# Performance work log

Hardware: AMD Instinct MI355X
Metric: run time of the kernel (lower is better)

## Reference

```python
import jax, jax.numpy as jnp
from jax import lax
import numpy as np

BATCH, SEQ_LEN, ENC_IN, C_OUT = 16, 512, 32, 32
N_ORDER = 256           # window_size
MULTISCALE = (1, 2, 4)
MODES = min(32, SEQ_LEN // 2)  # = 32


def make_hippo(N, dt):
    """HiPPO-LegT transition, bilinear (Tustin) discretization, Legendre eval matrix."""
    Q = np.arange(N, dtype=np.float64)
    R = (2 * Q + 1)[:, None]
    j, i = np.meshgrid(Q, Q)
    A = np.where(i < j, -1.0, (-1.0) ** (i - j + 1)) * R
    B = (-1.0) ** Q[:, None] * R                      # [N,1]
    I = np.eye(N)
    M = I - (dt / 2.0) * A
    Ad = np.linalg.solve(M, I + (dt / 2.0) * A)
    Bd = np.linalg.solve(M, dt * B).squeeze(-1)       # [N]
    vals = np.arange(0.0, 1.0, dt)
    x = 1.0 - 2.0 * vals
    P = np.zeros((N, len(vals)))
    P[0] = 1.0
    if N > 1:
        P[1] = x
    for n in range(1, N - 1):
        P[n + 1] = ((2 * n + 1) * x * P[n] - n * P[n - 1]) / (n + 1)
    E = P.T                                           # [len(vals), N]
    return Ad.astype(np.float32), Bd.astype(np.float32), E.astype(np.float32)


def setup_inputs():
    key = jax.random.key(0)
    ks = jax.random.split(key, 12)
    inp = {}
    inp['x_enc'] = jax.random.normal(ks[0], (BATCH, SEQ_LEN, ENC_IN), jnp.float32)
    inp['x_mark_enc'] = jax.random.normal(ks[1], (BATCH, SEQ_LEN, 4), jnp.float32)
    inp['x_dec'] = jax.random.normal(ks[2], (BATCH, SEQ_LEN, ENC_IN), jnp.float32)
    inp['x_mark_dec'] = jax.random.normal(ks[3], (BATCH, SEQ_LEN, 4), jnp.float32)
    inp['affine_weight'] = jnp.ones((1, 1, ENC_IN), jnp.float32)
    inp['affine_bias'] = jnp.zeros((1, 1, ENC_IN), jnp.float32)
    scale = 1.0 / (N_ORDER * N_ORDER)
    for s in range(3):
        inp[f'wr{s}'] = scale * jax.random.uniform(ks[4 + 2 * s], (N_ORDER, N_ORDER, MODES), jnp.float32)
        inp[f'wi{s}'] = scale * jax.random.uniform(ks[5 + 2 * s], (N_ORDER, N_ORDER, MODES), jnp.float32)
    inp['mlp_w'] = 0.1 * jax.random.normal(ks[10], (1, 3), jnp.float32)
    inp['mlp_b'] = jnp.zeros((1,), jnp.float32)
    inp['proj_w'] = 0.02 * jax.random.normal(ks[11], (ENC_IN, C_OUT), jnp.float32)
    inp['proj_b'] = jnp.zeros((C_OUT,), jnp.float32)
    for s, m in enumerate(MULTISCALE):
        A, Bv, E = make_hippo(N_ORDER, 1.0 / SEQ_LEN / m)
        inp[f'A{s}'] = jnp.asarray(A)
        inp[f'Bv{s}'] = jnp.asarray(Bv)
        inp[f'E{s}'] = jnp.asarray(E)
    return inp


def _hippo_scan(x, A, Bv):
    # x: [B, L, C] -> cs: [L, B, C, N]; c_t = A c_{t-1} + B f_t (applied on last dim)
    B_, L, C = x.shape
    c0 = jnp.zeros((B_, C, A.shape[0]), x.dtype)
    At = A.T
    def step(c, f):                      # f: [B, C]
        c = c @ At + f[..., None] * Bv
        return c, c
    _, cs = lax.scan(step, c0, jnp.transpose(x, (1, 0, 2)))
    return cs


def _spectral_conv(xc, wr, wi):
    # xc: [B, C, N, L]; keep first MODES rfft bins, complex channel mix over N, irfft
    L = xc.shape[-1]
    xf = jnp.fft.rfft(xc)                                # [B,C,N,L//2+1] complex64
    W = (wr + 1j * wi).astype(jnp.complex64)             # [N,N,MODES]
    out = jnp.einsum('bjix,iox->bjox', xf[..., :MODES], W)
    out_ft = jnp.pad(out, ((0, 0), (0, 0), (0, 0), (0, L // 2 + 1 - MODES)))
    return jnp.fft.irfft(out_ft, n=L)                    # [B,C,N,L]


def _forward(x_enc, affine_weight, affine_bias, specs, mlp_w, mlp_b, proj_w, proj_b, hippos):
    means = lax.stop_gradient(jnp.mean(x_enc, axis=1, keepdims=True))
    xc = x_enc - means
    stdev = lax.stop_gradient(jnp.sqrt(jnp.var(xc, axis=1, keepdims=True) + 1e-5))
    x = xc / stdev
    x = x * affine_weight + affine_bias                  # [B, L, C]
    pred_len = SEQ_LEN
    decs = []
    for (wr, wi), (A, Bv, E) in zip(specs, hippos):
        # multiscale slice x[:, -m*pred_len:] clips to full seq_len since pred_len==seq_len
        cs = _hippo_scan(x, A, Bv)                       # [L,B,C,N]
        x_in_c = jnp.transpose(cs, (1, 2, 3, 0))         # [B,C,N,L]
        out1 = _spectral_conv(x_in_c, wr, wi)            # [B,C,N,L]
        x_dec_c = out1[..., pred_len - 1]                # [B,C,N]
        dec = x_dec_c @ E[-pred_len:, :].T               # [B,C,pred_len]
        decs.append(dec)
    stacked = jnp.stack(decs, axis=-1)                   # [B,C,P,3]
    y = stacked @ mlp_w[0] + mlp_b[0]                    # Linear(3,1) + squeeze -> [B,C,P]
    y = jnp.transpose(y, (0, 2, 1))                      # [B,P,C]
    y = (y - affine_bias) / (affine_weight + 1e-10)
    y = y * stdev + means
    return y @ proj_w + proj_b                           # OutputBlock: per-step channel projection


def reference(x_enc, x_mark_enc, x_dec, x_mark_dec, affine_weight, affine_bias,
              wr0, wi0, wr1, wi1, wr2, wi2, mlp_w, mlp_b, proj_w, proj_b,
              A0, Bv0, E0, A1, Bv1, E1, A2, Bv2, E2):
    specs = [(wr0, wi0), (wr1, wi1), (wr2, wi2)]
    hippos = [(A0, Bv0, E0), (A1, Bv1, E1), (A2, Bv2, E2)]
    return _forward(x_enc, affine_weight, affine_bias, specs, mlp_w, mlp_b, proj_w, proj_b, hippos)
```

## Files before the change

### kernel.cpp

```cpp
#include <hip/hip_runtime.h>
#include <math.h>

#define SEQ 512
#define NORD 256
#define MODES 32
#define KBIG (NORD*MODES*2)
#define PI_F 3.14159265358979323846f

typedef _Float16 half8 __attribute__((ext_vector_type(8)));
typedef float floatx4 __attribute__((ext_vector_type(4)));


struct GJob {
  const float* A; const float* B; float* C; const float* scale_ptr;
  int M, N, lda, k0, k1, atomic;
};
struct GJobs { GJob j[6]; };

__global__ __launch_bounds__(256) void gemm32_k(GJobs P) {
  GJob jb = P.j[blockIdx.z];
  int col0 = blockIdx.x * 32;
  int row0 = blockIdx.y * 32;
  if (row0 >= jb.M || col0 >= jb.N) return;
  __shared__ float As[64][34];
  __shared__ float Bs[64][36];
  int tid = threadIdx.x;
  int tx = tid & 15, ty = tid >> 4;
  const float* A = jb.A; const float* B = jb.B;
  int M = jb.M, N = jb.N, lda = jb.lda;
  int kcA = (tid & 15) * 4, rA = tid >> 4;
  int ccB = (tid & 7) * 4, kkB = tid >> 3;
  int gr0 = row0 + rA, gr1 = row0 + rA + 16;
  const float4 z4 = make_float4(0.f, 0.f, 0.f, 0.f);
  float4 a0, a1, b0, b1;
  {
    int kb = jb.k0;
    a0 = (gr0 < M) ? *(const float4*)&A[(size_t)gr0 * lda + kb + kcA] : z4;
    a1 = (gr1 < M) ? *(const float4*)&A[(size_t)gr1 * lda + kb + kcA] : z4;
    b0 = *(const float4*)&B[(size_t)(kb + kkB) * N + col0 + ccB];
    b1 = *(const float4*)&B[(size_t)(kb + kkB + 32) * N + col0 + ccB];
  }
  float acc00 = 0.f, acc01 = 0.f, acc10 = 0.f, acc11 = 0.f;
  for (int kb = jb.k0; kb < jb.k1; kb += 64) {
    As[kcA+0][rA] = a0.x; As[kcA+1][rA] = a0.y; As[kcA+2][rA] = a0.z; As[kcA+3][rA] = a0.w;
    As[kcA+0][rA+16] = a1.x; As[kcA+1][rA+16] = a1.y; As[kcA+2][rA+16] = a1.z; As[kcA+3][rA+16] = a1.w;
    *(float4*)&Bs[kkB][ccB] = b0;
    *(float4*)&Bs[kkB+32][ccB] = b1;
    __syncthreads();
    if (kb + 64 < jb.k1) {
      int kn = kb + 64;
      a0 = (gr0 < M) ? *(const float4*)&A[(size_t)gr0 * lda + kn + kcA] : z4;
      a1 = (gr1 < M) ? *(const float4*)&A[(size_t)gr1 * lda + kn + kcA] : z4;
      b0 = *(const float4*)&B[(size_t)(kn + kkB) * N + col0 + ccB];
      b1 = *(const float4*)&B[(size_t)(kn + kkB + 32) * N + col0 + ccB];
    }
    #pragma unroll
    for (int k = 0; k < 64; k++) {
      float2 av = *(float2*)&As[k][ty * 2];
      float2 bv = *(float2*)&Bs[k][tx * 2];
      acc00 += av.x * bv.x; acc01 += av.x * bv.y;
      acc10 += av.y * bv.x; acc11 += av.y * bv.y;
    }
    __syncthreads();
  }
  float sc = jb.scale_ptr ? *jb.scale_ptr : 1.f;
  int gr = row0 + ty * 2, gc = col0 + tx * 2;
  float v00 = acc00 * sc, v01 = acc01 * sc, v10 = acc10 * sc, v11 = acc11 * sc;
  if (jb.atomic) {
    if (gr < M)     { atomicAdd(&jb.C[(size_t)gr * N + gc], v00);     atomicAdd(&jb.C[(size_t)gr * N + gc + 1], v01); }
    if (gr + 1 < M) { atomicAdd(&jb.C[(size_t)(gr+1) * N + gc], v10); atomicAdd(&jb.C[(size_t)(gr+1) * N + gc + 1], v11); }
  } else {
    if (gr < M)     { jb.C[(size_t)gr * N + gc] = v00;     jb.C[(size_t)gr * N + gc + 1] = v01; }
    if (gr + 1 < M) { jb.C[(size_t)(gr+1) * N + gc] = v10; jb.C[(size_t)(gr+1) * N + gc + 1] = v11; }
  }
}


__global__ __launch_bounds__(256) void prep_k(const float* A0, const float* A1, const float* A2,
                                              const float* B0, const float* B1, const float* B2,
                                              const float* E0, const float* E1, const float* E2,
                                              float* R, float* Kry, float* Et, float* Z) {
  long bid = blockIdx.x;
  if (bid < 768) {
    long idx = bid * 256 + threadIdx.x;
    int scl = (int)(idx >> 16);
    int r = (int)(idx & 65535);
    int m = r >> 8, i2 = r & 255;
    const float* A = scl == 0 ? A0 : (scl == 1 ? A1 : A2);
    R[(size_t)scl * 2 * 65536 + (size_t)m * 256 + i2] = A[(size_t)i2 * 256 + m];
  } else if (bid < 2304) {
    long idx = (bid - 768) * 256 + threadIdx.x;
    int scl = (int)(idx / 131072);
    int r = (int)(idx % 131072);
    int p = r >> 8, o = r & 255;
    const float* E; int rows;
    if (scl == 0) { E = E0; rows = 512; }
    else if (scl == 1) { E = E1; rows = 1024; }
    else { E = E2; rows = 2048; }
    int base = rows - 512;
    Et[(size_t)scl * 131072 + (size_t)o * 512 + p] = E[(size_t)(base + p) * 256 + o];
  } else if (bid < 2307) {
    int scl = (int)(bid - 2304);
    const float* B = scl == 0 ? B0 : (scl == 1 ? B1 : B2);
    Kry[(size_t)scl * 512 * 256 + threadIdx.x] = B[threadIdx.x];
  } else {
    long idx = (bid - 2307) * 256 + threadIdx.x;
    if (idx < 655360) Z[idx] = 0.f;
  }
}


__global__ __launch_bounds__(256) void revin_k(const float* __restrict__ x,
                                               const float* __restrict__ aw,
                                               const float* __restrict__ ab,
                                               float* __restrict__ F,
                                               float* __restrict__ stats) {
  int row = blockIdx.x;
  int b = row >> 5, c = row & 31;
  int tid = threadIdx.x;
  const float* xp = x + (size_t)b * SEQ * 32 + c;
  float v0 = xp[(size_t)tid * 32];
  float v1 = xp[(size_t)(tid + 256) * 32];
  float s = v0 + v1, s2 = v0 * v0 + v1 * v1;
  for (int off = 32; off; off >>= 1) {
    s  += __shfl_down(s,  off, 64);
    s2 += __shfl_down(s2, off, 64);
  }
  __shared__ float ws1[4], ws2[4];
  __shared__ float mean_s, istd_s;
  int wid = tid >> 6, lane = tid & 63;
  if (lane == 0) { ws1[wid] = s; ws2[wid] = s2; }
  __syncthreads();
  if (tid == 0) {
    float t1 = ws1[0] + ws1[1] + ws1[2] + ws1[3];
    float t2 = ws2[0] + ws2[1] + ws2[2] + ws2[3];
    float mean = t1 / 512.f;
    float var = t2 / 512.f - mean * mean;
    float sd = sqrtf(var + 1e-5f);
    mean_s = mean; istd_s = 1.f / sd;
    stats[row] = mean; stats[512 + row] = sd;
  }
  __syncthreads();
  float w = aw[c], bb = ab[c];
  float m = mean_s, is = istd_s;
  F[(size_t)row * SEQ + tid]       = (v0 - m) * is * w + bb;
  F[(size_t)row * SEQ + tid + 256] = (v1 - m) * is * w + bb;
}


__global__ __launch_bounds__(256) void qbuildA_k(const float* __restrict__ Kry,
                                                 float2* __restrict__ Pp, int s0) {
  int bg = blockIdx.x;
  int s = s0 + (bg >> 8);
  int r = bg & 255;
  int k = r & 31, c = r >> 5;
  const float* Kry_s = Kry + (size_t)s * 131072;
  float2* P = Pp + (size_t)s * 65536;
  int i = threadIdx.x;
  float ar = 0.f, ai = 0.f;
  const float step = 2.f * PI_F / 512.f;
  int m0 = c * 64;
  for (int mm = 0; mm < 64; mm++) {
    int m = m0 + mm;
    float kap = Kry_s[(size_t)m * 256 + i];
    float sn, cn; __sincosf(step * (float)((k * m) & 511), &sn, &cn);
    ar += kap * cn; ai -= kap * sn;
  }
  P[(size_t)(c * 32 + k) * 256 + i] = make_float2(ar, ai);
}

__global__ __launch_bounds__(256) void qbuildB_k(const float* __restrict__ Kry,
                                                 const float2* __restrict__ Pp,
                                                 _Float16* __restrict__ Qf, int s0) {
  int bg = blockIdx.x;
  int slab = bg >> 8;
  int s = s0 + slab;
  int r = bg & 255;
  int ig = r & 31, c = r >> 5;
  const float* Kry_s = Kry + (size_t)s * 131072;
  const float2* P = Pp + (size_t)s * 65536;
  uint4* Qd4 = (uint4*)(Qf + (size_t)slab * 8388608);
  int tid = threadIdx.x;
  int k = tid & 31, il = tid >> 5;
  int i = ig * 8 + il;
  __shared__ __align__(16) unsigned int buf[16 * 260];
  float ar = 0.f, ai = 0.f;
  for (int cp = 0; cp < c; cp++) {
    float2 p = P[(size_t)(cp * 32 + k) * 256 + i];
    ar += p.x; ai += p.y;
  }
  const float step = 2.f * PI_F / 512.f;
  int m0 = c * 64;
  int st_low = tid & 15;
  int part_base = tid >> 4;
  for (int mb = 0; mb < 64; mb += 16) {
    #pragma unroll
    for (int mm = 0; mm < 16; mm++) {
      int m = m0 + mb + mm;
      float kap = Kry_s[(size_t)m * 256 + i];
      float sn, cn; __sincosf(step * (float)((k * m) & 511), &sn, &cn);
      ar += kap * cn; ai -= kap * sn;
      int st = 511 - m;
      float sn2, cn2; __sincosf(step * (float)((k * st) & 511), &sn2, &cn2);
      float qr = ar * cn2 + ai * sn2;
      float qi = ai * cn2 - ar * sn2;
      qr = fminf(fmaxf(qr, -60000.f), 60000.f);
      qi = fminf(fmaxf(qi, -60000.f), 60000.f);
      _Float16 h0 = (_Float16)qr, h1 = (_Float16)qi;
      unsigned short u0, u1;
      __builtin_memcpy(&u0, &h0, 2); __builtin_memcpy(&u1, &h1, 2);
      buf[(st & 15) * 260 + il * 32 + k] = (unsigned int)u0 | ((unsigned int)u1 << 16);
    }
    __syncthreads();
    int st_base = 496 - m0 - mb;
    int st = st_base + st_low;
    size_t rowbase = (size_t)(st >> 4) * 512;
    #pragma unroll
    for (int p = 0; p < 4; p++) {
      int part = part_base + p * 16;
      int ilw = part >> 3, k4 = part & 7;
      int iw = ig * 8 + ilw;
      size_t g = (rowbase + (size_t)(iw * 2 + (k4 >> 2))) * 64
               + (size_t)((k4 & 3) * 16 + st_low);
      Qd4[g] = *(const uint4*)&buf[st_low * 260 + ilw * 32 + k4 * 4];
    }
    __syncthreads();
  }
}


__global__ __launch_bounds__(256) void wbigT_k(const float* wr0, const float* wi0,
                                               const float* wr1, const float* wi1,
                                               const float* wr2, const float* wi2,
                                               _Float16* __restrict__ Wt, int s0) {
  int bg = blockIdx.x;
  int slab = bg >> 8;
  int s = s0 + slab;
  int r = bg & 255;
  int og = r >> 3, iq = r & 7;
  const float* wr = s == 0 ? wr0 : (s == 1 ? wr1 : wr2);
  const float* wi = s == 0 ? wi0 : (s == 1 ? wi1 : wi2);
  unsigned int* Wd = (unsigned int*)(Wt + (size_t)slab * 4194304);
  int tid = threadIdx.x;
  int ol = tid >> 5, k = tid & 31;
  int o = og * 8 + ol;
  float sn, cn; __sincosf((2.f * PI_F / 512.f) * (float)k, &sn, &cn);
  float g = ((k == 0) ? (1.f / 512.f) : (2.f / 512.f)) * 4096.f;
  float gc = g * cn, gs = g * sn;
  size_t obase = (size_t)(o >> 4) * 512;
  int osub = (((k >> 2) & 3) * 16 + (o & 15)) * 4 + (k & 3);
  for (int ii = 0; ii < 32; ii++) {
    int i = iq * 32 + ii;
    float a = wr[(size_t)i * 8192 + o * 32 + k];
    float b = wi[(size_t)i * 8192 + o * 32 + k];
    float v0 = gc * a + gs * b;
    float v1 = gs * a - gc * b;
    _Float16 h0 = (_Float16)v0, h1 = (_Float16)v1;
    unsigned short u0, u1;
    __builtin_memcpy(&u0, &h0, 2); __builtin_memcpy(&u1, &h1, 2);
    Wd[(obase + (size_t)(i * 2 + (k >> 4))) * 256 + osub] = (unsigned int)u0 | ((unsigned int)u1 << 16);
  }
}


__global__ __launch_bounds__(256) void umfma_k(const _Float16* __restrict__ Qf,
                                               const _Float16* __restrict__ Wt,
                                               float* __restrict__ U, int s0) {
  int kslab = blockIdx.x;
  int y = blockIdx.y;
  int slab = blockIdx.z;
  int s = s0 + slab;
  int mtile = y >> 1, nh = y & 1;
  const _Float16* Q = Qf + (size_t)slab * 8388608;
  const _Float16* W = Wt + (size_t)slab * 4194304;
  float* Us = U + (size_t)s * 131072;
  int tid = threadIdx.x;
  int w = tid >> 6, lane = tid & 63;
  int wm = w >> 1, wn = w & 1;
  int quad = lane >> 4, lm = lane & 15;
  int mt0 = mtile * 4 + wm * 2;
  int nt0 = nh * 8 + wn * 4;
  int kt0 = kslab * 32;
  const _Float16* qa = Q + (((size_t)mt0 * 512 + (size_t)kt0) * 64 + (size_t)lane) * 8;
  const _Float16* wb = W + (((size_t)nt0 * 512 + (size_t)kt0) * 64 + (size_t)lane) * 8;
  floatx4 acc[2][4];
  #pragma unroll
  for (int a = 0; a < 2; a++)
    #pragma unroll
    for (int b = 0; b < 4; b++) acc[a][b] = (floatx4)(0.f);

#define QA(mi, kk) (*(const half8*)(qa + (size_t)(mi) * 262144 + (size_t)(kk) * 512))
#define WB(ni, kk) (*(const half8*)(wb + (size_t)(ni) * 262144 + (size_t)(kk) * 512))
#define MFMA8(A0, A1, B0, B1, B2, B3) \
  acc[0][0] = __builtin_amdgcn_mfma_f32_16x16x32_f16(A0, B0, acc[0][0], 0, 0, 0); \
  acc[0][1] = __builtin_amdgcn_mfma_f32_16x16x32_f16(A0, B1, acc[0][1], 0, 0, 0); \
  acc[0][2] = __builtin_amdgcn_mfma_f32_16x16x32_f16(A0, B2, acc[0][2], 0, 0, 0); \
  acc[0][3] = __builtin_amdgcn_mfma_f32_16x16x32_f16(A0, B3, acc[0][3], 0, 0, 0); \
  acc[1][0] = __builtin_amdgcn_mfma_f32_16x16x32_f16(A1, B0, acc[1][0], 0, 0, 0); \
  acc[1][1] = __builtin_amdgcn_mfma_f32_16x16x32_f16(A1, B1, acc[1][1], 0, 0, 0); \
  acc[1][2] = __builtin_amdgcn_mfma_f32_16x16x32_f16(A1, B2, acc[1][2], 0, 0, 0); \
  acc[1][3] = __builtin_amdgcn_mfma_f32_16x16x32_f16(A1, B3, acc[1][3], 0, 0, 0);

  half8 aA0 = QA(0, 0), aA1 = QA(1, 0);
  half8 bA0 = WB(0, 0), bA1 = WB(1, 0), bA2 = WB(2, 0), bA3 = WB(3, 0);
  half8 aB0, aB1, bB0, bB1, bB2, bB3;
  for (int kt = 0; kt < 30; kt += 2) {
    aB0 = QA(0, kt + 1); aB1 = QA(1, kt + 1);
    bB0 = WB(0, kt + 1); bB1 = WB(1, kt + 1); bB2 = WB(2, kt + 1); bB3 = WB(3, kt + 1);
    MFMA8(aA0, aA1, bA0, bA1, bA2, bA3);
    aA0 = QA(0, kt + 2); aA1 = QA(1, kt + 2);
    bA0 = WB(0, kt + 2); bA1 = WB(1, kt + 2); bA2 = WB(2, kt + 2); bA3 = WB(3, kt + 2);
    MFMA8(aB0, aB1, bB0, bB1, bB2, bB3);
  }
  aB0 = QA(0, 31); aB1 = QA(1, 31);
  bB0 = WB(0, 31); bB1 = WB(1, 31); bB2 = WB(2, 31); bB3 = WB(3, 31);
  MFMA8(aA0, aA1, bA0, bA1, bA2, bA3);
  MFMA8(aB0, aB1, bB0, bB1, bB2, bB3);
#undef QA
#undef WB
#undef MFMA8

  const float sc = 1.f / 4096.f;
  #pragma unroll
  for (int mi = 0; mi < 2; mi++) {
    int R0 = (mt0 + mi) * 16 + quad * 4;
    #pragma unroll
    for (int ni = 0; ni < 4; ni++) {
      int gc = (nt0 + ni) * 16 + lm;
      #pragma unroll
      for (int rr2 = 0; rr2 < 4; rr2++)
        atomicAdd(&Us[(size_t)(R0 + rr2) * 256 + gc], acc[mi][ni][rr2] * sc);
    }
  }
}


__global__ __launch_bounds__(256) void final_k(const float* __restrict__ y0,
                                               const float* __restrict__ stats,
                                               const float* __restrict__ aw,
                                               const float* __restrict__ ab,
                                               const float* __restrict__ mlp_b,
                                               const float* __restrict__ pw,
                                               const float* __restrict__ pb,
                                               float* __restrict__ out) {
  int b = blockIdx.y;
  int p0 = blockIdx.x * 8;
  int tid = threadIdx.x;
  __shared__ float ys[32 * 8];
  __shared__ float pws[32 * 32];
  for (int t = tid; t < 1024; t += 256) pws[t] = pw[t];
  int c = tid >> 3, pl = tid & 7;
  int row = b * 32 + c;
  float mean = stats[row], sd = stats[512 + row];
  float raw = y0[(size_t)row * 512 + p0 + pl];
  float v = ((raw + mlp_b[0]) - ab[c]) / (aw[c] + 1e-10f) * sd + mean;
  ys[c * 8 + pl] = v;
  __syncthreads();
  int co = tid & 31; int pl2 = tid >> 5;
  float accv = pb[co];
  #pragma unroll
  for (int cc = 0; cc < 32; cc++) accv += ys[cc * 8 + pl2] * pws[cc * 32 + co];
  out[(size_t)b * 512 * 32 + (size_t)(p0 + pl2) * 32 + co] = accv;
}


extern "C" void kernel_launch(void* const* d_in, const int* in_sizes, int n_in,
                              void* d_out, int out_size, void* d_ws, size_t ws_size,
                              hipStream_t stream) {
  const float* x_enc = (const float*)d_in[0];
  const float* aw = (const float*)d_in[4];
  const float* ab = (const float*)d_in[5];
  const float* wr[3] = {(const float*)d_in[6], (const float*)d_in[8], (const float*)d_in[10]};
  const float* wi[3] = {(const float*)d_in[7], (const float*)d_in[9], (const float*)d_in[11]};
  const float* mlp_w = (const float*)d_in[12];
  const float* mlp_b = (const float*)d_in[13];
  const float* proj_w = (const float*)d_in[14];
  const float* proj_b = (const float*)d_in[15];
  const float* Am[3]  = {(const float*)d_in[16], (const float*)d_in[19], (const float*)d_in[22]};
  const float* Bv[3]  = {(const float*)d_in[17], (const float*)d_in[20], (const float*)d_in[23]};
  const float* Em[3]  = {(const float*)d_in[18], (const float*)d_in[21], (const float*)d_in[24]};

  float* w = (float*)d_ws;
  float* F     = w; w += 512 * 512;
  float* stats = w; w += 1024;
  float* Kry   = w; w += 3 * 512 * 256;
  float* R     = w; w += 3 * 2 * 65536;
  float* U     = w; w += 3 * 512 * 256;
  float* Ttot  = w; w += 512 * 512;
  float* Et    = w; w += 3 * 256 * 512;
  float* y0    = w; w += 512 * 512;
  float* Pp    = w; w += 3 * 65536 * 2;
  _Float16* Qf = (_Float16*)w;

  size_t base_bytes = (size_t)((char*)Qf - (char*)d_ws);
  size_t slab_bytes = (size_t)(8388608 + 4194304) * 2;
  int nS = (ws_size >= base_bytes + 3 * slab_bytes) ? 3 : 1;
  _Float16* Wb = Qf + (size_t)nS * 8388608;

  revin_k<<<512, 256, 0, stream>>>(x_enc, aw, ab, F, stats);
  prep_k<<<4867, 256, 0, stream>>>(Am[0], Am[1], Am[2], Bv[0], Bv[1], Bv[2],
                                   Em[0], Em[1], Em[2], R, Kry, Et, U);

  for (int j = 0; j < 9; j++) {
    GJobs P{};
    int M = 1 << j;
    int cur = j & 1;
    int nz = 0;
    for (int s = 0; s < 3; s++) {
      float* Ks = Kry + (size_t)s * 131072;
      float* Rj = R + (size_t)s * 131072 + (size_t)cur * 65536;
      float* Rn = R + (size_t)s * 131072 + (size_t)(1 - cur) * 65536;
      P.j[nz++] = {Ks, Rj, Ks + (size_t)M * 256, nullptr, M, 256, 256, 0, 256, 0};
      if (j < 8) P.j[nz++] = {Rj, Rj, Rn, nullptr, 256, 256, 256, 0, 256, 0};
    }
    gemm32_k<<<dim3(8, 8, nz), 256, 0, stream>>>(P);
  }

  if (nS == 3) {
    qbuildA_k<<<768, 256, 0, stream>>>(Kry, (float2*)Pp, 0);
    qbuildB_k<<<768, 256, 0, stream>>>(Kry, (const float2*)Pp, Qf, 0);
    wbigT_k<<<768, 256, 0, stream>>>(wr[0], wi[0], wr[1], wi[1], wr[2], wi[2], Wb, 0);
    umfma_k<<<dim3(16, 16, 3), 256, 0, stream>>>(Qf, Wb, U, 0);
  } else {
    for (int s = 0; s < 3; s++) {
      qbuildA_k<<<256, 256, 0, stream>>>(Kry, (float2*)Pp, s);
      qbuildB_k<<<256, 256, 0, stream>>>(Kry, (const float2*)Pp, Qf, s);
      wbigT_k<<<256, 256, 0, stream>>>(wr[0], wi[0], wr[1], wi[1], wr[2], wi[2], Wb, s);
      umfma_k<<<dim3(16, 16, 1), 256, 0, stream>>>(Qf, Wb, U, s);
    }
  }

  {
    GJobs P{};
    for (int s = 0; s < 3; s++)
      P.j[s] = {U + (size_t)s * 131072, Et + (size_t)s * 131072, Ttot,
                mlp_w + s, 512, 512, 256, 0, 256, 1};
    gemm32_k<<<dim3(16, 16, 3), 256, 0, stream>>>(P);
  }

  {
    GJobs P{};
    P.j[0] = {F, Ttot, y0, nullptr, 512, 512, 512, 0, 512, 0};
    gemm32_k<<<dim3(16, 16, 1), 256, 0, stream>>>(P);
  }

  final_k<<<dim3(64, 16), 256, 0, stream>>>(y0, stats, aw, ab, mlp_b, proj_w, proj_b,
                                            (float*)d_out);
}
```

Measured before the change: 363.6 us.

## Merge prep kernels, tile transposes, fuse qbuildA with wbigT, LDS-stage umfma

Folds revin into the prep kernel and turns the per-element transposes of A and E into 32x32 shared-memory tiled transposes, with float4 zero-fill. The Fourier-projection build (qbuildA) and the weight conversion (wbigT) now run as one launch over concatenated block ranges. The MFMA GEMM now stages Q and W tiles into LDS with double-buffered global_load_lds instead of loading fragments straight from global memory into registers. The aim is fewer launches, coalesced transposes and overlap of loads with MFMA, at the cost of extra LDS use and a barrier on every k-step.

```diff
diff --git a/kernel.cpp b/kernel.cpp
--- a/kernel.cpp
+++ b/kernel.cpp
@@ -76,98 +76,99 @@
 }
 
 
-__global__ __launch_bounds__(256) void prep_k(const float* A0, const float* A1, const float* A2,
-                                              const float* B0, const float* B1, const float* B2,
-                                              const float* E0, const float* E1, const float* E2,
-                                              float* R, float* Kry, float* Et, float* Z) {
-  long bid = blockIdx.x;
-  if (bid < 768) {
-    long idx = bid * 256 + threadIdx.x;
-    int scl = (int)(idx >> 16);
-    int r = (int)(idx & 65535);
-    int m = r >> 8, i2 = r & 255;
+__global__ __launch_bounds__(256) void prep2_k(const float* __restrict__ x_enc,
+                                               const float* __restrict__ aw,
+                                               const float* __restrict__ ab,
+                                               float* __restrict__ F,
+                                               float* __restrict__ stats,
+                                               const float* A0, const float* A1, const float* A2,
+                                               const float* B0, const float* B1, const float* B2,
+                                               const float* E0, const float* E1, const float* E2,
+                                               float* R, float* Kry, float* Et, float* Z) {
+  __shared__ float tile[32][33];
+  __shared__ float ws1[4], ws2[4];
+  __shared__ float mean_s, istd_s;
+  int bid = blockIdx.x;
+  int tid = threadIdx.x;
+  if (bid < 512) {
+    int row = bid;
+    int b = row >> 5, c = row & 31;
+    const float* xp = x_enc + (size_t)b * SEQ * 32 + c;
+    float v0 = xp[(size_t)tid * 32];
+    float v1 = xp[(size_t)(tid + 256) * 32];
+    float s = v0 + v1, s2 = v0 * v0 + v1 * v1;
+    for (int off = 32; off; off >>= 1) {
+      s  += __shfl_down(s,  off, 64);
+      s2 += __shfl_down(s2, off, 64);
+    }
+    int wid = tid >> 6, lane = tid & 63;
+    if (lane == 0) { ws1[wid] = s; ws2[wid] = s2; }
+    __syncthreads();
+    if (tid == 0) {
+      float t1 = ws1[0] + ws1[1] + ws1[2] + ws1[3];
+      float t2 = ws2[0] + ws2[1] + ws2[2] + ws2[3];
+      float mean = t1 / 512.f;
+      float var = t2 / 512.f - mean * mean;
+      float sd = sqrtf(var + 1e-5f);
+      mean_s = mean; istd_s = 1.f / sd;
+      stats[row] = mean; stats[512 + row] = sd;
+    }
+    __syncthreads();
+    float w = aw[c], bb = ab[c];
+    float m = mean_s, is = istd_s;
+    F[(size_t)row * SEQ + tid]       = (v0 - m) * is * w + bb;
+    F[(size_t)row * SEQ + tid + 256] = (v1 - m) * is * w + bb;
+  } else if (bid < 704) {
+    int b2 = bid - 512;
+    int scl = b2 >> 6, t = b2 & 63;
+    int ti = t >> 3, tm = t & 7;
     const float* A = scl == 0 ? A0 : (scl == 1 ? A1 : A2);
-    R[(size_t)scl * 2 * 65536 + (size_t)m * 256 + i2] = A[(size_t)i2 * 256 + m];
-  } else if (bid < 2304) {
-    long idx = (bid - 768) * 256 + threadIdx.x;
-    int scl = (int)(idx / 131072);
-    int r = (int)(idx % 131072);
-    int p = r >> 8, o = r & 255;
+    float* Rd = R + (size_t)scl * 2 * 65536;
+    int tx = tid & 31, ty0 = tid >> 5;
+    int i0 = ti * 32, m0 = tm * 32;
+    #pragma unroll
+    for (int r = 0; r < 4; r++) {
+      int ty = ty0 + r * 8;
+      tile[ty][tx] = A[(size_t)(i0 + ty) * 256 + m0 + tx];
+    }
+    __syncthreads();
+    #pragma unroll
+    for (int r = 0; r < 4; r++) {
+      int ty = ty0 + r * 8;
+      Rd[(size_t)(m0 + ty) * 256 + i0 + tx] = tile[tx][ty];
+    }
+  } else if (bid < 1088) {
+    int b2 = bid - 704;
+    int scl = b2 >> 7, t = b2 & 127;
+    int tp = t >> 3, to = t & 7;
     const float* E; int rows;
     if (scl == 0) { E = E0; rows = 512; }
     else if (scl == 1) { E = E1; rows = 1024; }
     else { E = E2; rows = 2048; }
     int base = rows - 512;
-    Et[(size_t)scl * 131072 + (size_t)o * 512 + p] = E[(size_t)(base + p) * 256 + o];
-  } else if (bid < 2307) {
-    int scl = (int)(bid - 2304);
+    int p0 = tp * 32, o0 = to * 32;
+    int tx = tid & 31, ty0 = tid >> 5;
+    #pragma unroll
+    for (int r = 0; r < 4; r++) {
+      int ty = ty0 + r * 8;
+      tile[ty][tx] = E[(size_t)(base + p0 + ty) * 256 + o0 + tx];
+    }
+    __syncthreads();
+    #pragma unroll
+    for (int r = 0; r < 4; r++) {
+      int ty = ty0 + r * 8;
+      Et[(size_t)scl * 131072 + (size_t)(o0 + ty) * 512 + p0 + tx] = tile[tx][ty];
+    }
+  } else if (bid < 1091) {
+    int scl = bid - 1088;
     const float* B = scl == 0 ? B0 : (scl == 1 ? B1 : B2);
-    Kry[(size_t)scl * 512 * 256 + threadIdx.x] = B[threadIdx.x];
+    Kry[(size_t)scl * 512 * 256 + tid] = B[tid];
   } else {
-    long idx = (bid - 2307) * 256 + threadIdx.x;
-    if (idx < 655360) Z[idx] = 0.f;
-  }
-}
-
-
-__global__ __launch_bounds__(256) void revin_k(const float* __restrict__ x,
-                                               const float* __restrict__ aw,
-                                               const float* __restrict__ ab,
-                                               float* __restrict__ F,
-                                               float* __restrict__ stats) {
-  int row = blockIdx.x;
-  int b = row >> 5, c = row & 31;
-  int tid = threadIdx.x;
-  const float* xp = x + (size_t)b * SEQ * 32 + c;
-  float v0 = xp[(size_t)tid * 32];
-  float v1 = xp[(size_t)(tid + 256) * 32];
-  float s = v0 + v1, s2 = v0 * v0 + v1 * v1;
-  for (int off = 32; off; off >>= 1) {
-    s  += __shfl_down(s,  off, 64);
-    s2 += __shfl_down(s2, off, 64);
-  }
-  __shared__ float ws1[4], ws2[4];
-  __shared__ float mean_s, istd_s;
-  int wid = tid >> 6, lane = tid & 63;
-  if (lane == 0) { ws1[wid] = s; ws2[wid] = s2; }
-  __syncthreads();
-  if (tid == 0) {
-    float t1 = ws1[0] + ws1[1] + ws1[2] + ws1[3];
-    float t2 = ws2[0] + ws2[1] + ws2[2] + ws2[3];
-    float mean = t1 / 512.f;
-    float var = t2 / 512.f - mean * mean;
-    float sd = sqrtf(var + 1e-5f);
-    mean_s = mean; istd_s = 1.f / sd;
-    stats[row] = mean; stats[512 + row] = sd;
-  }
-  __syncthreads();
-  float w = aw[c], bb = ab[c];
-  float m = mean_s, is = istd_s;
-  F[(size_t)row * SEQ + tid]       = (v0 - m) * is * w + bb;
-  F[(size_t)row * SEQ + tid + 256] = (v1 - m) * is * w + bb;
-}
-
-
-__global__ __launch_bounds__(256) void qbuildA_k(const float* __restrict__ Kry,
-                                                 float2* __restrict__ Pp, int s0) {
-  int bg = blockIdx.x;
-  int s = s0 + (bg >> 8);
-  int r = bg & 255;
-  int k = r & 31, c = r >> 5;
-  const float* Kry_s = Kry + (size_t)s * 131072;
-  float2* P = Pp + (size_t)s * 65536;
-  int i = threadIdx.x;
-  float ar = 0.f, ai = 0.f;
-  const float step = 2.f * PI_F / 512.f;
-  int m0 = c * 64;
-  for (int mm = 0; mm < 64; mm++) {
-    int m = m0 + mm;
-    float kap = Kry_s[(size_t)m * 256 + i];
-    float sn, cn; __sincosf(step * (float)((k * m) & 511), &sn, &cn);
-    ar += kap * cn; ai -= kap * sn;
-  }
-  P[(size_t)(c * 32 + k) * 256 + i] = make_float2(ar, ai);
-}
+    int idx = (bid - 1091) * 256 + tid;
+    ((float4*)Z)[idx] = make_float4(0.f, 0.f, 0.f, 0.f);
+  }
+}
+
 
 __global__ __launch_bounds__(256) void qbuildB_k(const float* __restrict__ Kry,
                                                  const float2* __restrict__ Pp,
@@ -229,36 +230,59 @@
 }
 
 
-__global__ __launch_bounds__(256) void wbigT_k(const float* wr0, const float* wi0,
-                                               const float* wr1, const float* wi1,
-                                               const float* wr2, const float* wi2,
-                                               _Float16* __restrict__ Wt, int s0) {
-  int bg = blockIdx.x;
-  int slab = bg >> 8;
-  int s = s0 + slab;
-  int r = bg & 255;
-  int og = r >> 3, iq = r & 7;
-  const float* wr = s == 0 ? wr0 : (s == 1 ? wr1 : wr2);
-  const float* wi = s == 0 ? wi0 : (s == 1 ? wi1 : wi2);
-  unsigned int* Wd = (unsigned int*)(Wt + (size_t)slab * 4194304);
-  int tid = threadIdx.x;
-  int ol = tid >> 5, k = tid & 31;
-  int o = og * 8 + ol;
-  float sn, cn; __sincosf((2.f * PI_F / 512.f) * (float)k, &sn, &cn);
-  float g = ((k == 0) ? (1.f / 512.f) : (2.f / 512.f)) * 4096.f;
-  float gc = g * cn, gs = g * sn;
-  size_t obase = (size_t)(o >> 4) * 512;
-  int osub = (((k >> 2) & 3) * 16 + (o & 15)) * 4 + (k & 3);
-  for (int ii = 0; ii < 32; ii++) {
-    int i = iq * 32 + ii;
-    float a = wr[(size_t)i * 8192 + o * 32 + k];
-    float b = wi[(size_t)i * 8192 + o * 32 + k];
-    float v0 = gc * a + gs * b;
-    float v1 = gs * a - gc * b;
-    _Float16 h0 = (_Float16)v0, h1 = (_Float16)v1;
-    unsigned short u0, u1;
-    __builtin_memcpy(&u0, &h0, 2); __builtin_memcpy(&u1, &h1, 2);
-    Wd[(obase + (size_t)(i * 2 + (k >> 4))) * 256 + osub] = (unsigned int)u0 | ((unsigned int)u1 << 16);
+__global__ __launch_bounds__(256) void qw_k(const float* __restrict__ Kry,
+                                            float2* __restrict__ Pp,
+                                            const float* wr0, const float* wi0,
+                                            const float* wr1, const float* wi1,
+                                            const float* wr2, const float* wi2,
+                                            _Float16* __restrict__ Wt, int s0, int nA) {
+  int bid = blockIdx.x;
+  int tid = threadIdx.x;
+  if (bid < nA) {
+    int bg = bid;
+    int s = s0 + (bg >> 8);
+    int r = bg & 255;
+    int k = r & 31, c = r >> 5;
+    const float* Kry_s = Kry + (size_t)s * 131072;
+    float2* P = Pp + (size_t)s * 65536;
+    int i = tid;
+    float ar = 0.f, ai = 0.f;
+    const float step = 2.f * PI_F / 512.f;
+    int m0 = c * 64;
+    for (int mm = 0; mm < 64; mm++) {
+      int m = m0 + mm;
+      float kap = Kry_s[(size_t)m * 256 + i];
+      float sn, cn; __sincosf(step * (float)((k * m) & 511), &sn, &cn);
+      ar += kap * cn; ai -= kap * sn;
+    }
+    P[(size_t)(c * 32 + k) * 256 + i] = make_float2(ar, ai);
+  } else {
+    int bg = bid - nA;
+    int slab = bg >> 8;
+    int s = s0 + slab;
+    int r = bg & 255;
+    int og = r >> 3, iq = r & 7;
+    const float* wr = s == 0 ? wr0 : (s == 1 ? wr1 : wr2);
+    const float* wi = s == 0 ? wi0 : (s == 1 ? wi1 : wi2);
+    unsigned int* Wd = (unsigned int*)(Wt + (size_t)slab * 4194304);
+    int ol = tid >> 5, k = tid & 31;
+    int o = og * 8 + ol;
+    float sn, cn; __sincosf((2.f * PI_F / 512.f) * (float)k, &sn, &cn);
+    float g = ((k == 0) ? (1.f / 512.f) : (2.f / 512.f)) * 4096.f;
+    float gc = g * cn, gs = g * sn;
+    size_t obase = (size_t)(o >> 4) * 512;
+    int osub = (((k >> 2) & 3) * 16 + (o & 15)) * 4 + (k & 3);
+    for (int ii = 0; ii < 32; ii++) {
+      int i = iq * 32 + ii;
+      float a = wr[(size_t)i * 8192 + o * 32 + k];
+      float b = wi[(size_t)i * 8192 + o * 32 + k];
+      float v0 = gc * a + gs * b;
+      float v1 = gs * a - gc * b;
+      _Float16 h0 = (_Float16)v0, h1 = (_Float16)v1;
+      unsigned short u0, u1;
+      __builtin_memcpy(&u0, &h0, 2); __builtin_memcpy(&u1, &h1, 2);
+      Wd[(obase + (size_t)(i * 2 + (k >> 4))) * 256 + osub] = (unsigned int)u0 | ((unsigned int)u1 << 16);
+    }
   }
 }
 
@@ -266,11 +290,12 @@
 __global__ __launch_bounds__(256) void umfma_k(const _Float16* __restrict__ Qf,
                                                const _Float16* __restrict__ Wt,
                                                float* __restrict__ U, int s0) {
+  __shared__ __align__(16) _Float16 lds[2][12288];
   int kslab = blockIdx.x;
   int y = blockIdx.y;
   int slab = blockIdx.z;
   int s = s0 + slab;
-  int mtile = y >> 1, nh = y & 1;
+  int mtb = y >> 1, ntb = y & 1;
   const _Float16* Q = Qf + (size_t)slab * 8388608;
   const _Float16* W = Wt + (size_t)slab * 4194304;
   float* Us = U + (size_t)s * 131072;
@@ -278,58 +303,73 @@
   int w = tid >> 6, lane = tid & 63;
   int wm = w >> 1, wn = w & 1;
   int quad = lane >> 4, lm = lane & 15;
-  int mt0 = mtile * 4 + wm * 2;
-  int nt0 = nh * 8 + wn * 4;
-  int kt0 = kslab * 32;
-  const _Float16* qa = Q + (((size_t)mt0 * 512 + (size_t)kt0) * 64 + (size_t)lane) * 8;
-  const _Float16* wb = W + (((size_t)nt0 * 512 + (size_t)kt0) * 64 + (size_t)lane) * 8;
+  int mt0g = mtb * 4;
+  int nt0g = ntb * 8;
+  int ktg0 = kslab * 32;
+  size_t laneoff = (size_t)lane * 8;
+
   floatx4 acc[2][4];
   #pragma unroll
   for (int a = 0; a < 2; a++)
     #pragma unroll
     for (int b = 0; b < 4; b++) acc[a][b] = (floatx4)(0.f);
 
-#define QA(mi, kk) (*(const half8*)(qa + (size_t)(mi) * 262144 + (size_t)(kk) * 512))
-#define WB(ni, kk) (*(const half8*)(wb + (size_t)(ni) * 262144 + (size_t)(kk) * 512))
-#define MFMA8(A0, A1, B0, B1, B2, B3) \
-  acc[0][0] = __builtin_amdgcn_mfma_f32_16x16x32_f16(A0, B0, acc[0][0], 0, 0, 0); \
-  acc[0][1] = __builtin_amdgcn_mfma_f32_16x16x32_f16(A0, B1, acc[0][1], 0, 0, 0); \
-  acc[0][2] = __builtin_amdgcn_mfma_f32_16x16x32_f16(A0, B2, acc[0][2], 0, 0, 0); \
-  acc[0][3] = __builtin_amdgcn_mfma_f32_16x16x32_f16(A0, B3, acc[0][3], 0, 0, 0); \
-  acc[1][0] = __builtin_amdgcn_mfma_f32_16x16x32_f16(A1, B0, acc[1][0], 0, 0, 0); \
-  acc[1][1] = __builtin_amdgcn_mfma_f32_16x16x32_f16(A1, B1, acc[1][1], 0, 0, 0); \
-  acc[1][2] = __builtin_amdgcn_mfma_f32_16x16x32_f16(A1, B2, acc[1][2], 0, 0, 0); \
-  acc[1][3] = __builtin_amdgcn_mfma_f32_16x16x32_f16(A1, B3, acc[1][3], 0, 0, 0);
-
-  half8 aA0 = QA(0, 0), aA1 = QA(1, 0);
-  half8 bA0 = WB(0, 0), bA1 = WB(1, 0), bA2 = WB(2, 0), bA3 = WB(3, 0);
-  half8 aB0, aB1, bB0, bB1, bB2, bB3;
-  for (int kt = 0; kt < 30; kt += 2) {
-    aB0 = QA(0, kt + 1); aB1 = QA(1, kt + 1);
-    bB0 = WB(0, kt + 1); bB1 = WB(1, kt + 1); bB2 = WB(2, kt + 1); bB3 = WB(3, kt + 1);
-    MFMA8(aA0, aA1, bA0, bA1, bA2, bA3);
-    aA0 = QA(0, kt + 2); aA1 = QA(1, kt + 2);
-    bA0 = WB(0, kt + 2); bA1 = WB(1, kt + 2); bA2 = WB(2, kt + 2); bA3 = WB(3, kt + 2);
-    MFMA8(aB0, aB1, bB0, bB1, bB2, bB3);
-  }
-  aB0 = QA(0, 31); aB1 = QA(1, 31);
-  bB0 = WB(0, 31); bB1 = WB(1, 31); bB2 = WB(2, 31); bB3 = WB(3, 31);
-  MFMA8(aA0, aA1, bA0, bA1, bA2, bA3);
-  MFMA8(aB0, aB1, bB0, bB1, bB2, bB3);
-#undef QA
-#undef WB
-#undef MFMA8
+  auto stage = [&](int ks, int bufi) {
+    int ktg = ktg0 + ks * 2;
+    #pragma unroll
+    for (int q = 0; q < 6; q++) {
+      int f = w * 6 + q;
+      const _Float16* src;
+      if (f < 8) {
+        src = Q + (((size_t)(mt0g + (f >> 1)) * 512) + (size_t)(ktg + (f & 1))) * 512;
+      } else {
+        int g = f - 8;
+        src = W + (((size_t)(nt0g + (g >> 1)) * 512) + (size_t)(ktg + (g & 1))) * 512;
+      }
+      __builtin_amdgcn_global_load_lds(
+          (const __attribute__((address_space(1))) unsigned int*)(src + laneoff),
+          (__attribute__((address_space(3))) unsigned int*)&lds[bufi][f * 512],
+          16, 0, 0);
+    }
+  };
+
+  stage(0, 0);
+  __syncthreads();
+  int buf = 0;
+  for (int ks = 0; ks < 16; ks++) {
+    if (ks < 15) stage(ks + 1, buf ^ 1);
+    half8 a[2][2], b[4][2];
+    #pragma unroll
+    for (int mi2 = 0; mi2 < 2; mi2++)
+      #pragma unroll
+      for (int kk = 0; kk < 2; kk++)
+        a[mi2][kk] = *(const half8*)&lds[buf][(size_t)(((wm * 2 + mi2) * 2 + kk) * 512) + laneoff];
+    #pragma unroll
+    for (int ni2 = 0; ni2 < 4; ni2++)
+      #pragma unroll
+      for (int kk = 0; kk < 2; kk++)
+        b[ni2][kk] = *(const half8*)&lds[buf][(size_t)(4096 + ((wn * 4 + ni2) * 2 + kk) * 512) + laneoff];
+    #pragma unroll
+    for (int kk = 0; kk < 2; kk++)
+      #pragma unroll
+      for (int mi2 = 0; mi2 < 2; mi2++)
+        #pragma unroll
+        for (int ni2 = 0; ni2 < 4; ni2++)
+          acc[mi2][ni2] = __builtin_amdgcn_mfma_f32_16x16x32_f16(a[mi2][kk], b[ni2][kk], acc[mi2][ni2], 0, 0, 0);
+    __syncthreads();
+    buf ^= 1;
+  }
 
   const float sc = 1.f / 4096.f;
   #pragma unroll
-  for (int mi = 0; mi < 2; mi++) {
-    int R0 = (mt0 + mi) * 16 + quad * 4;
-    #pragma unroll
-    for (int ni = 0; ni < 4; ni++) {
-      int gc = (nt0 + ni) * 16 + lm;
+  for (int mi2 = 0; mi2 < 2; mi2++) {
+    int R0 = (mt0g + wm * 2 + mi2) * 16 + quad * 4;
+    #pragma unroll
+    for (int ni2 = 0; ni2 < 4; ni2++) {
+      int gc = (nt0g + wn * 4 + ni2) * 16 + lm;
       #pragma unroll
       for (int rr2 = 0; rr2 < 4; rr2++)
-        atomicAdd(&Us[(size_t)(R0 + rr2) * 256 + gc], acc[mi][ni][rr2] * sc);
+        atomicAdd(&Us[(size_t)(R0 + rr2) * 256 + gc], acc[mi2][ni2][rr2] * sc);
     }
   }
 }
@@ -397,9 +437,9 @@
   int nS = (ws_size >= base_bytes + 3 * slab_bytes) ? 3 : 1;
   _Float16* Wb = Qf + (size_t)nS * 8388608;
 
-  revin_k<<<512, 256, 0, stream>>>(x_enc, aw, ab, F, stats);
-  prep_k<<<4867, 256, 0, stream>>>(Am[0], Am[1], Am[2], Bv[0], Bv[1], Bv[2],
-                                   Em[0], Em[1], Em[2], R, Kry, Et, U);
+  prep2_k<<<1731, 256, 0, stream>>>(x_enc, aw, ab, F, stats,
+                                    Am[0], Am[1], Am[2], Bv[0], Bv[1], Bv[2],
+                                    Em[0], Em[1], Em[2], R, Kry, Et, U);
 
   for (int j = 0; j < 9; j++) {
     GJobs P{};
@@ -417,15 +457,15 @@
   }
 
   if (nS == 3) {
-    qbuildA_k<<<768, 256, 0, stream>>>(Kry, (float2*)Pp, 0);
+    qw_k<<<1536, 256, 0, stream>>>(Kry, (float2*)Pp, wr[0], wi[0], wr[1], wi[1],
+                                   wr[2], wi[2], Wb, 0, 768);
     qbuildB_k<<<768, 256, 0, stream>>>(Kry, (const float2*)Pp, Qf, 0);
-    wbigT_k<<<768, 256, 0, stream>>>(wr[0], wi[0], wr[1], wi[1], wr[2], wi[2], Wb, 0);
     umfma_k<<<dim3(16, 16, 3), 256, 0, stream>>>(Qf, Wb, U, 0);
   } else {
     for (int s = 0; s < 3; s++) {
-      qbuildA_k<<<256, 256, 0, stream>>>(Kry, (float2*)Pp, s);
+      qw_k<<<512, 256, 0, stream>>>(Kry, (float2*)Pp, wr[0], wi[0], wr[1], wi[1],
+                                    wr[2], wi[2], Wb, s, 256);
       qbuildB_k<<<256, 256, 0, stream>>>(Kry, (const float2*)Pp, Qf, s);
-      wbigT_k<<<256, 256, 0, stream>>>(wr[0], wi[0], wr[1], wi[1], wr[2], wi[2], Wb, s);
       umfma_k<<<dim3(16, 16, 1), 256, 0, stream>>>(Qf, Wb, U, s);
     }
   }
```

Result: faster. 351.8 us (-3.2%).
